# Performance work log

Measured on AMD Instinct MI355X. Metric: run time of the kernel, lower is better.

## Reference

```python
import jax, jax.numpy as jnp
import numpy as np

IMG = 640
C = 256
A = 9
NC = 80
K = 1000          # max candidates kept into NMS (fixed for jit)
SCORE_TH = 0.05
IOU_TH = 0.5
STRIDES = (8, 16, 32, 64, 128)
SIZES = (32, 64, 128, 256, 512)


def conv3(x, w, b):
    # x: [N,C,H,W], w: [O,I,3,3]
    y = jax.lax.conv_general_dilated(x, w, (1, 1), 'SAME',
                                     dimension_numbers=('NCHW', 'OIHW', 'NCHW'))
    return y + b[None, :, None, None]


def head(x, ws, bs, hw, hb):
    for i in range(4):
        x = jax.nn.relu(conv3(x, ws[i], bs[i]))
    return conv3(x, hw, hb)


def classifier(x, ws, bs, hw, hb):
    y = jax.nn.sigmoid(head(x, ws, bs, hw, hb))          # [N, A*NC, H, W]
    n, _, h, w = y.shape
    y = y.transpose(0, 2, 3, 1).reshape(n, h, w, A, NC)  # NHWA,NC ordering as in torch view
    return y.reshape(n, -1, NC)


def regressor(x, ws, bs, hw, hb):
    y = head(x, ws, bs, hw, hb)                           # [N, A*4, H, W]
    n, _, h, w = y.shape
    return y.transpose(0, 2, 3, 1).reshape(n, -1, 4)


def make_anchors():
    ratios = jnp.array([0.5, 1.0, 2.0], jnp.float32)
    scales = jnp.array([1.0, 2.0 ** (1.0 / 3.0), 2.0 ** (2.0 / 3.0)], jnp.float32)
    levels = []
    for stride, size in zip(STRIDES, SIZES):
        ws = (size * scales[None, :]) / jnp.sqrt(ratios[:, None])  # [3,3]
        hs = (size * scales[None, :]) * jnp.sqrt(ratios[:, None])
        ws, hs = ws.reshape(-1), hs.reshape(-1)                    # [9]
        fs = IMG // stride
        c = (jnp.arange(fs, dtype=jnp.float32) + 0.5) * stride
        cy, cx = jnp.meshgrid(c, c, indexing='ij')                 # [H,W]
        cx, cy = cx[..., None], cy[..., None]                      # [H,W,1]
        boxes = jnp.stack([cx - ws / 2, cy - hs / 2, cx + ws / 2, cy + hs / 2], -1)  # [H,W,9,4]
        levels.append(boxes.reshape(-1, 4))
    return jnp.concatenate(levels, 0)  # [76725, 4]


def decode_clip(anchors, loc):
    # BBoxTransform with std (0.1,0.1,0.2,0.2), then ClipBoxes to image
    w = anchors[:, 2] - anchors[:, 0]
    h = anchors[:, 3] - anchors[:, 1]
    cx = anchors[:, 0] + 0.5 * w
    cy = anchors[:, 1] + 0.5 * h
    dx, dy = loc[:, 0] * 0.1, loc[:, 1] * 0.1
    dw, dh = loc[:, 2] * 0.2, loc[:, 3] * 0.2
    pcx, pcy = cx + dx * w, cy + dy * h
    pw, ph = jnp.exp(dw) * w, jnp.exp(dh) * h
    boxes = jnp.stack([pcx - 0.5 * pw, pcy - 0.5 * ph, pcx + 0.5 * pw, pcy + 0.5 * ph], -1)
    return jnp.clip(boxes, 0.0, float(IMG))


def nms_keep(boxes, valid):
    # boxes [K,4] sorted by descending score, valid [K] bool; greedy NMS keep mask
    x1, y1, x2, y2 = boxes[:, 0], boxes[:, 1], boxes[:, 2], boxes[:, 3]
    area = jnp.maximum(x2 - x1, 0.0) * jnp.maximum(y2 - y1, 0.0)
    xx1 = jnp.maximum(x1[:, None], x1[None, :])
    yy1 = jnp.maximum(y1[:, None], y1[None, :])
    xx2 = jnp.minimum(x2[:, None], x2[None, :])
    yy2 = jnp.minimum(y2[:, None], y2[None, :])
    inter = jnp.maximum(xx2 - xx1, 0.0) * jnp.maximum(yy2 - yy1, 0.0)
    iou = inter / (area[:, None] + area[None, :] - inter + 1e-8)
    idx = jnp.arange(boxes.shape[0])

    def body(i, keep):
        sup = (iou[i] > IOU_TH) & (idx > i) & keep[i]
        return keep & ~sup

    return jax.lax.fori_loop(0, boxes.shape[0], body, valid)


def forward(p3, p4, p5, p6, p7, cls_w, cls_b, cls_hw, cls_hb, reg_w, reg_b, reg_hw, reg_hb):
    feats = [p3, p4, p5, p6, p7]
    cls_pred = jnp.concatenate([classifier(f, cls_w, cls_b, cls_hw, cls_hb) for f in feats], 1)[0]  # [N_anch, NC]
    loc_pred = jnp.concatenate([regressor(f, reg_w, reg_b, reg_hw, reg_hb) for f in feats], 1)[0]   # [N_anch, 4]
    anchors = make_anchors()
    boxes = decode_clip(anchors, loc_pred)
    scores = jnp.max(cls_pred, axis=1)                     # [N_anch]
    masked = jnp.where(scores > SCORE_TH, scores, -1.0)
    top_vals, top_idx = jax.lax.top_k(masked, K)
    valid = top_vals > 0.0
    sel_boxes = boxes[top_idx]                             # [K,4]
    keep = nms_keep(sel_boxes, valid)
    sel_cls = cls_pred[top_idx]                            # [K,NC]
    nms_scores = jnp.where(keep, top_vals, 0.0)
    nms_classes = jnp.argmax(sel_cls, axis=1).astype(jnp.int32)
    nms_boxes = jnp.where(keep[:, None], sel_boxes, 0.0)
    return nms_scores, nms_classes, nms_boxes, keep


def setup_inputs() -> dict:
    key = jax.random.key(0)
    ks = jax.random.split(key, 12)
    inp = {}
    for i, (name, hw_) in enumerate(zip(['p3', 'p4', 'p5', 'p6', 'p7'], [80, 40, 20, 10, 5])):
        inp[name] = jax.random.normal(ks[i], (1, C, hw_, hw_), jnp.float32)
    inp['cls_w'] = jax.random.normal(ks[5], (4, C, C, 3, 3), jnp.float32) * 0.05
    inp['cls_b'] = jnp.zeros((4, C), jnp.float32)
    inp['cls_hw'] = jax.random.normal(ks[6], (A * NC, C, 3, 3), jnp.float32) * 0.05
    inp['cls_hb'] = jnp.full((A * NC,), -2.0, jnp.float32)
    inp['reg_w'] = jax.random.normal(ks[7], (4, C, C, 3, 3), jnp.float32) * 0.05
    inp['reg_b'] = jnp.zeros((4, C), jnp.float32)
    inp['reg_hw'] = jax.random.normal(ks[8], (36, C, 3, 3), jnp.float32) * 0.05
    inp['reg_hb'] = jnp.zeros((36,), jnp.float32)
    return inp


def reference(p3, p4, p5, p6, p7, cls_w, cls_b, cls_hw, cls_hb, reg_w, reg_b, reg_hw, reg_hb):
    return forward(p3, p4, p5, p6, p7, cls_w, cls_b, cls_hw, cls_hb, reg_w, reg_b, reg_hw, reg_hb)
```

## Files before the change

kernel.cpp:

```cpp
#include <hip/hip_runtime.h>
#include <math.h>
#include <stdint.h>

#define NANCH 76725
#define NPAD  131072
#define NPAD2 32768
#define PXTOT 8525

typedef _Float16 half8 __attribute__((ext_vector_type(8)));
typedef _Float16 half4 __attribute__((ext_vector_type(4)));
typedef float float4v __attribute__((ext_vector_type(4)));
typedef unsigned long long u64;

#define ACT2_EL  ((size_t)PXTOT * 512)
#define HEADC_EL (720 * PXTOT)
#define HEADR_EL (36 * PXTOT)

#define TRUNK_WP_EL (9 * 2 * 8 * 16 * 64 * 8)
#define CLSH_WP_EL  (9 * 2 * 8 * 48 * 64 * 8)
#define REGH_WP_EL  (9 * 2 * 8 * 4 * 64 * 8)

struct PrepArgs {
    const float* src[10];
    _Float16*    dst[10];
    int Co[10], NC16[10];
    long base[11];
};

__global__ __launch_bounds__(256) void prep_k(PrepArgs P)
{
    long idx = (long)blockIdx.x * 256 + threadIdx.x;
    if (idx >= P.base[10]) return;
    int e = 0;
    while (idx >= P.base[e + 1]) e++;
    long local = idx - P.base[e];
    const int NC16 = P.NC16[e], Co = P.Co[e];
    int lane = (int)(local & 63);
    long t2 = local >> 6;
    int c16 = (int)(t2 % NC16);
    long t3 = t2 / NC16;
    int cc = (int)(t3 & 7);
    int t4 = (int)(t3 >> 3);
    int s = t4 & 1, tap = t4 >> 1;
    int co = c16 * 16 + (lane & 15);
    int kb = cc * 32 + (lane >> 4) * 8;
    const float* src = P.src[e];
    half8 out;
#pragma unroll
    for (int j = 0; j < 8; j++) {
        float v = (co < Co) ? src[(size_t)(co * 256 + kb + j) * 9 + tap] : 0.f;
        _Float16 h = (_Float16)v;
        out[j] = s ? (_Float16)(v - (float)h) : h;
    }
    _Float16* dst = P.dst[e] + ((((size_t)(tap * 2 + s) * 8 + cc) * NC16 + c16) * 64 + lane) * 8;
    *(half8*)dst = out;
}

struct RepArgs { const float* src[5]; _Float16* dst; };

__global__ __launch_bounds__(256) void repack_k(RepArgs R)
{
    __shared__ float T[64][257];
    const int cumT[5] = {100, 125, 132, 134, 135};
    const int Wt[5]   = {80, 40, 20, 10, 5};
    const int pxB[5]  = {0, 6400, 8000, 8400, 8500};
    int t = blockIdx.x;
    int lv = 0; while (t >= cumT[lv]) lv++;
    int tile = t - (lv ? cumT[lv - 1] : 0);
    const int HW = Wt[lv] * Wt[lv];
    const int pxStart = tile * 64;
    const float* src = R.src[lv];
    const int tid = threadIdx.x, w = tid >> 6, l6 = tid & 63;
    int p = pxStart + l6;
    bool ok = p < HW;
    for (int ci = w; ci < 256; ci += 4)
        T[l6][ci] = ok ? src[(size_t)ci * HW + p] : 0.f;
    __syncthreads();
    _Float16* dst = R.dst + (size_t)pxB[lv] * 512;
    for (int px = w; px < 64; px += 4) {
        int pp = pxStart + px;
        if (pp >= HW) continue;
        half4 h, l;
#pragma unroll
        for (int j = 0; j < 4; j++) {
            float v = T[px][l6 * 4 + j];
            _Float16 hh = (_Float16)v;
            h[j] = hh; l[j] = (_Float16)(v - (float)hh);
        }
        *(half4*)(dst + (size_t)pp * 512 + l6 * 4) = h;
        *(half4*)(dst + (size_t)pp * 512 + 256 + l6 * 4) = l;
    }
}

struct C3Args {
    const _Float16* aIn0; const _Float16* aIn1;
    _Float16* aOut0; _Float16* aOut1;
    float* hOut0; float* hOut1;
    const _Float16* wp0; const _Float16* wp1;
    const float* bias0; const float* bias1;
    int CoPad0, CoPad1, Co0, Co1, mode;
};

__global__ __launch_bounds__(256, 4) void conv3_k(C3Args A)
{
    const int cumT[5] = {200, 250, 265, 271, 273};
    const int txA[5]  = {10, 5, 3, 2, 1};
    const int Wt[5]   = {80, 40, 20, 10, 5};
    const int pxB[5]  = {0, 6400, 8000, 8400, 8500};

    __shared__ __align__(16) _Float16 Xs[60 * 72];

    const int gid = blockIdx.x;
    int head, coGrp, t;
    if (A.mode == 0) {
        int oct = gid & 7; head = oct >> 2; int tq = oct & 3;
        int p = gid >> 3; coGrp = p & 1; int tl = p >> 1;
        t = tq * 69 + tl;
    } else {
        int oct = gid & 7; int tq = oct & 3; int ch = oct >> 2;
        int p = gid >> 3; int ci = p & 3; int tl = p >> 2;
        int combo = ch * 4 + ci;
        if (combo >= 7) return;
        head = (combo == 6) ? 1 : 0;
        coGrp = (combo == 6) ? 0 : combo;
        t = tq * 69 + tl;
    }
    if (t >= 273) return;

    int lv = 0; while (t >= cumT[lv]) lv++;
    const int tile = t - (lv ? cumT[lv - 1] : 0);
    const int W = Wt[lv], HW = W * W;
    const int tx = txA[lv];
    const int tyi = tile / tx, txi = tile - tyi * tx;
    const int x0 = txi * 8, y0 = tyi * 4;

    const _Float16* aIn = (head ? A.aIn1 : A.aIn0) + (size_t)pxB[lv] * 512;
    const _Float16* wp  = head ? A.wp1 : A.wp0;
    const float* bias   = head ? A.bias1 : A.bias0;
    const int CoPad     = head ? A.CoPad1 : A.CoPad0;
    const int Co        = head ? A.Co1 : A.Co0;
    const int NC16      = CoPad >> 4;

    const int tid = threadIdx.x;
    const int w = tid >> 6, lane = tid & 63;
    const int l15 = lane & 15, quad = lane >> 4;
    const int coW = coGrp * 128 + w * 32;
    const bool active = coW < CoPad;
    const int c16b = coW >> 4;

    float4v acc[2][2];
#pragma unroll
    for (int i = 0; i < 2; i++)
#pragma unroll
        for (int j = 0; j < 2; j++) acc[i][j] = (float4v){0.f, 0.f, 0.f, 0.f};

    const half8 z8 = {(_Float16)0, (_Float16)0, (_Float16)0, (_Float16)0,
                      (_Float16)0, (_Float16)0, (_Float16)0, (_Float16)0};

    for (int cc = 0; cc < 8; cc++) {
        const int ci0 = cc * 32;
        __syncthreads();
        {
            int u0 = tid, u1 = tid + 256;
            int px0 = u0 >> 3, sg0 = u0 & 7;
            int r0 = px0 / 10, c0 = px0 - r0 * 10;
            int gy0 = y0 + r0 - 1, gx0 = x0 + c0 - 1;
            bool v0ok = (gy0 >= 0) && (gy0 < W) && (gx0 >= 0) && (gx0 < W);
            int e0 = (sg0 < 4) ? (ci0 + sg0 * 8) : (256 + ci0 + (sg0 - 4) * 8);
            int gp0 = v0ok ? (gy0 * W + gx0) : 0;
            half8 v0 = v0ok ? *(const half8*)(aIn + (size_t)gp0 * 512 + e0) : z8;

            bool u1v = u1 < 480;
            int px1 = u1 >> 3, sg1 = u1 & 7;
            int r1 = px1 / 10, c1 = px1 - r1 * 10;
            int gy1 = y0 + r1 - 1, gx1 = x0 + c1 - 1;
            bool v1ok = u1v && (gy1 >= 0) && (gy1 < W) && (gx1 >= 0) && (gx1 < W);
            int e1 = (sg1 < 4) ? (ci0 + sg1 * 8) : (256 + ci0 + (sg1 - 4) * 8);
            int gp1 = v1ok ? (gy1 * W + gx1) : 0;
            half8 v1 = v1ok ? *(const half8*)(aIn + (size_t)gp1 * 512 + e1) : z8;

            *(half8*)(Xs + px0 * 72 + sg0 * 8) = v0;
            if (u1v) *(half8*)(Xs + px1 * 72 + sg1 * 8) = v1;
        }
        __syncthreads();

        if (active) {
            for (int tap = 0; tap < 9; tap++) {
                const int dy = tap / 3 - 1, dx = tap % 3 - 1;
                half8 ah[2], al[2];
#pragma unroll
                for (int mf = 0; mf < 2; mf++) {
                    int lpx = (2 * mf + (l15 >> 3) + 1 + dy) * 10 + (l15 & 7) + 1 + dx;
                    const _Float16* lp = Xs + lpx * 72 + quad * 8;
                    ah[mf] = *(const half8*)lp;
                    al[mf] = *(const half8*)(lp + 32);
                }
                half8 bh[2], bl[2];
#pragma unroll
                for (int nf = 0; nf < 2; nf++) {
                    const _Float16* wb = wp +
                        ((((size_t)(tap * 2) * 8 + cc) * NC16 + c16b + nf) * 64 + lane) * 8;
                    bh[nf] = *(const half8*)wb;
                    bl[nf] = *(const half8*)(wb + (size_t)4096 * NC16);
                }
#pragma unroll
                for (int nf = 0; nf < 2; nf++) {
#pragma unroll
                    for (int mf = 0; mf < 2; mf++) {
                        acc[mf][nf] = __builtin_amdgcn_mfma_f32_16x16x32_f16(ah[mf], bh[nf], acc[mf][nf], 0, 0, 0);
                        acc[mf][nf] = __builtin_amdgcn_mfma_f32_16x16x32_f16(ah[mf], bl[nf], acc[mf][nf], 0, 0, 0);
                        acc[mf][nf] = __builtin_amdgcn_mfma_f32_16x16x32_f16(al[mf], bh[nf], acc[mf][nf], 0, 0, 0);
                    }
                }
            }
        }
    }

    if (!active) return;

    int coN[2];
    float bv[2];
#pragma unroll
    for (int nf = 0; nf < 2; nf++) {
        coN[nf] = coW + nf * 16 + l15;
        bv[nf] = (coN[nf] < Co) ? bias[coN[nf]] : 0.f;
    }

    if (A.mode == 0) {
        _Float16* ao = (head ? A.aOut1 : A.aOut0) + (size_t)pxB[lv] * 512;
#pragma unroll
        for (int nf = 0; nf < 2; nf++) {
#pragma unroll
            for (int mf = 0; mf < 2; mf++) {
#pragma unroll
                for (int r = 0; r < 4; r++) {
                    int m = quad * 4 + r;
                    int yy = y0 + 2 * mf + (m >> 3);
                    int xx = x0 + (m & 7);
                    if (yy < W && xx < W) {
                        int px = yy * W + xx;
                        float v = fmaxf(acc[mf][nf][r] + bv[nf], 0.f);
                        _Float16 h = (_Float16)v;
                        _Float16 lo = (_Float16)(v - (float)h);
                        ao[(size_t)px * 512 + coN[nf]] = h;
                        ao[(size_t)px * 512 + 256 + coN[nf]] = lo;
                    }
                }
            }
        }
    } else {
        float* ho = (head ? A.hOut1 : A.hOut0) + (size_t)Co * pxB[lv];
#pragma unroll
        for (int nf = 0; nf < 2; nf++) {
            if (coN[nf] < Co) {
                float* col = ho + (size_t)coN[nf] * HW;
#pragma unroll
                for (int mf = 0; mf < 2; mf++) {
#pragma unroll
                    for (int r = 0; r < 4; r++) {
                        int m = quad * 4 + r;
                        int yy = y0 + 2 * mf + (m >> 3);
                        int xx = x0 + (m & 7);
                        if (yy < W && xx < W) col[yy * W + xx] = acc[mf][nf][r] + bv[nf];
                    }
                }
            }
        }
    }
}

__global__ void cls_reduce_k(const float* __restrict__ ho,
                             u64* __restrict__ keys, int* __restrict__ cls_all)
{
    const int cumB[5] = {225, 282, 297, 301, 302};
    const int HWs[5]  = {6400, 1600, 400, 100, 25};
    const int pxB[5]  = {0, 6400, 8000, 8400, 8500};
    const int offs[5] = {0, 57600, 72000, 75600, 76500};
    int b = blockIdx.x;
    int lv = 0;
    while (b >= cumB[lv]) lv++;
    int local = (b - (lv ? cumB[lv - 1] : 0)) * 256 + threadIdx.x;
    const int HW = HWs[lv];
    if (local >= HW * 9) return;
    int a = local / HW, p = local - a * HW;
    const float* base = ho + (size_t)720 * pxB[lv] + (size_t)a * 80 * HW + p;
    float m = -1.f; int arg = 0;
    for (int c = 0; c < 80; c++) {
        float logit = base[(size_t)c * HW];
        float s = 1.0f / (1.0f + expf(-logit));
        if (s > m) { m = s; arg = c; }
    }
    float masked = (m > 0.05f) ? m : -1.0f;
    unsigned u = __float_as_uint(masked);
    unsigned su = (u & 0x80000000u) ? ~u : (u | 0x80000000u);
    int g = offs[lv] + p * 9 + a;
    keys[g] = ((u64)su << 32) | (u64)(0xFFFFFFFFu - (unsigned)g);
    cls_all[g] = arg;
}

struct DecArgs { float aw[45]; float ah[45]; };

__global__ void decode_k(const float* __restrict__ ro, DecArgs D, float* __restrict__ boxes_all)
{
    const int cumB[5] = {225, 282, 297, 301, 302};
    const int HWs[5]  = {6400, 1600, 400, 100, 25};
    const int Wt[5]   = {80, 40, 20, 10, 5};
    const int pxB[5]  = {0, 6400, 8000, 8400, 8500};
    const int offs[5] = {0, 57600, 72000, 75600, 76500};
    const float strd[5] = {8.f, 16.f, 32.f, 64.f, 128.f};
    int b = blockIdx.x;
    int lv = 0;
    while (b >= cumB[lv]) lv++;
    int local = (b - (lv ? cumB[lv - 1] : 0)) * 256 + threadIdx.x;
    const int HW = HWs[lv], W = Wt[lv];
    if (local >= HW * 9) return;
    int a = local / HW, p = local - a * HW;
    int y = p / W, x = p - y * W;
    float cx0 = ((float)x + 0.5f) * strd[lv];
    float cy0 = ((float)y + 0.5f) * strd[lv];
    float aw = D.aw[lv * 9 + a], ahh = D.ah[lv * 9 + a];
    float ax1 = cx0 - aw * 0.5f, ax2 = cx0 + aw * 0.5f;
    float ay1 = cy0 - ahh * 0.5f, ay2 = cy0 + ahh * 0.5f;
    float w = ax2 - ax1, h = ay2 - ay1;
    float cx = ax1 + 0.5f * w, cy = ay1 + 0.5f * h;
    const float* base = ro + (size_t)36 * pxB[lv] + p;
    float l0 = base[(size_t)(a * 4 + 0) * HW];
    float l1 = base[(size_t)(a * 4 + 1) * HW];
    float l2 = base[(size_t)(a * 4 + 2) * HW];
    float l3 = base[(size_t)(a * 4 + 3) * HW];
    float dx = l0 * 0.1f, dy = l1 * 0.1f, dw = l2 * 0.2f, dh = l3 * 0.2f;
    float pcx = cx + dx * w, pcy = cy + dy * h;
    float pw = expf(dw) * w, ph = expf(dh) * h;
    float bx1 = fminf(fmaxf(pcx - 0.5f * pw, 0.f), 640.f);
    float by1 = fminf(fmaxf(pcy - 0.5f * ph, 0.f), 640.f);
    float bx2 = fminf(fmaxf(pcx + 0.5f * pw, 0.f), 640.f);
    float by2 = fminf(fmaxf(pcy + 0.5f * ph, 0.f), 640.f);
    int g = offs[lv] + p * 9 + a;
    boxes_all[g * 4 + 0] = bx1;
    boxes_all[g * 4 + 1] = by1;
    boxes_all[g * 4 + 2] = bx2;
    boxes_all[g * 4 + 3] = by2;
}

__global__ void pad_keys_k(u64* __restrict__ keys)
{
    int i = blockIdx.x * blockDim.x + threadIdx.x + NANCH;
    if (i < NPAD) keys[i] = 0ULL;
}

__global__ __launch_bounds__(1024) void chunk_sort_desc_k(u64* __restrict__ keys)
{
    __shared__ u64 s[4096];
    const int base = blockIdx.x * 4096;
    for (int i = threadIdx.x; i < 4096; i += 1024) s[i] = keys[base + i];
    __syncthreads();
    for (int size = 2; size <= 4096; size <<= 1) {
        for (int stride = size >> 1; stride > 0; stride >>= 1) {
            for (int t = threadIdx.x; t < 2048; t += 1024) {
                int low = t & (stride - 1);
                int i = ((t - low) << 1) | low;
                int j = i + stride;
                bool desc = ((i & size) == 0);
                u64 a = s[i], b = s[j];
                if (desc ? (a < b) : (a > b)) { s[i] = b; s[j] = a; }
            }
            __syncthreads();
        }
    }
    for (int i = threadIdx.x; i < 4096; i += 1024) keys[base + i] = s[i];
}

__global__ __launch_bounds__(1024) void gather_top_k(const u64* __restrict__ keys,
                                                     u64* __restrict__ keys2)
{
    int i = blockIdx.x * 1024 + threadIdx.x;
    keys2[i] = keys[(i >> 10) * 4096 + (i & 1023)];
}

__global__ void bitonic_global_k(u64* __restrict__ keys, int size, int stride)
{
    int t = blockIdx.x * blockDim.x + threadIdx.x;
    int low = t & (stride - 1);
    int i = ((t - low) << 1) | low;
    int j = i + stride;
    bool desc = ((i & size) == 0);
    u64 a = keys[i], b = keys[j];
    if (desc ? (a < b) : (a > b)) { keys[i] = b; keys[j] = a; }
}

__global__ __launch_bounds__(1024) void bitonic_local_full_k(u64* __restrict__ keys)
{
    __shared__ u64 s[4096];
    const int base = blockIdx.x * 4096;
    for (int i = threadIdx.x; i < 4096; i += 1024) s[i] = keys[base + i];
    __syncthreads();
    for (int size = 2; size <= 4096; size <<= 1) {
        for (int stride = size >> 1; stride > 0; stride >>= 1) {
            for (int t = threadIdx.x; t < 2048; t += 1024) {
                int low = t & (stride - 1);
                int i = ((t - low) << 1) | low;
                int j = i + stride;
                bool desc = (((base + i) & size) == 0);
                u64 a = s[i], b = s[j];
                if (desc ? (a < b) : (a > b)) { s[i] = b; s[j] = a; }
            }
            __syncthreads();
        }
    }
    for (int i = threadIdx.x; i < 4096; i += 1024) keys[base + i] = s[i];
}

__global__ __launch_bounds__(1024) void bitonic_local_k(u64* __restrict__ keys, int size)
{
    __shared__ u64 s[4096];
    const int base = blockIdx.x * 4096;
    for (int i = threadIdx.x; i < 4096; i += 1024) s[i] = keys[base + i];
    __syncthreads();
    const bool desc = ((base & size) == 0);
    for (int stride = 2048; stride > 0; stride >>= 1) {
        for (int t = threadIdx.x; t < 2048; t += 1024) {
            int low = t & (stride - 1);
            int i = ((t - low) << 1) | low;
            int j = i + stride;
            u64 a = s[i], b = s[j];
            if (desc ? (a < b) : (a > b)) { s[i] = b; s[j] = a; }
        }
        __syncthreads();
    }
    for (int i = threadIdx.x; i < 4096; i += 1024) keys[base + i] = s[i];
}

__global__ void gather_cand_k(const u64* __restrict__ keys,
                              const float* __restrict__ boxes_all,
                              const int* __restrict__ cls_all,
                              float* __restrict__ cand)
{
    int i = blockIdx.x * 256 + threadIdx.x;
    if (i >= 1000) return;
    u64 k = keys[i];
    unsigned shi = (unsigned)(k >> 32);
    unsigned u = (shi & 0x80000000u) ? (shi ^ 0x80000000u) : ~shi;
    float val = __uint_as_float(u);
    int anchor = (int)(0xFFFFFFFFu - (unsigned)(k & 0xFFFFFFFFull));
    float x1 = boxes_all[anchor * 4 + 0];
    float y1 = boxes_all[anchor * 4 + 1];
    float x2 = boxes_all[anchor * 4 + 2];
    float y2 = boxes_all[anchor * 4 + 3];
    cand[i * 8 + 0] = x1;
    cand[i * 8 + 1] = y1;
    cand[i * 8 + 2] = x2;
    cand[i * 8 + 3] = y2;
    cand[i * 8 + 4] = fmaxf(x2 - x1, 0.f) * fmaxf(y2 - y1, 0.f);
    cand[i * 8 + 5] = val;
    cand[i * 8 + 6] = (float)cls_all[anchor];
    cand[i * 8 + 7] = (val > 0.0f) ? 1.f : 0.f;
}

__global__ __launch_bounds__(256) void iou_mask_k(const float* __restrict__ cand,
                                                  u64* __restrict__ mask)
{
    const int i = blockIdx.x;
    const float x1 = cand[i * 8 + 0], y1 = cand[i * 8 + 1];
    const float x2 = cand[i * 8 + 2], y2 = cand[i * 8 + 3];
    const float ar = cand[i * 8 + 4];
    const int tid = threadIdx.x;
    const int wave = tid >> 6, lane = tid & 63;
    for (int base = 0; base < 1024; base += 256) {
        int j = base + tid;
        bool sup = false;
        if (j < 1000 && j > i) {
            float jx1 = cand[j * 8 + 0], jy1 = cand[j * 8 + 1];
            float jx2 = cand[j * 8 + 2], jy2 = cand[j * 8 + 3];
            float jar = cand[j * 8 + 4];
            float xx1 = fmaxf(x1, jx1), yy1 = fmaxf(y1, jy1);
            float xx2 = fminf(x2, jx2), yy2 = fminf(y2, jy2);
            float inter = fmaxf(xx2 - xx1, 0.f) * fmaxf(yy2 - yy1, 0.f);
            float iou = inter / (ar + jar - inter + 1e-8f);
            sup = iou > 0.5f;
        }
        u64 ball = __ballot(sup);
        int word = (base >> 6) + wave;
        if (lane == 0) mask[(size_t)i * 16 + word] = ball;
    }
}

__global__ __launch_bounds__(256) void nms_sweep_out_k(const float* __restrict__ cand,
                                                       const u64* __restrict__ M,
                                                       float* __restrict__ out)
{
    __shared__ float C[1000 * 8];
    __shared__ int KPs[1000];
    const int tid = threadIdx.x;
    for (int i = tid; i < 8000; i += 256) C[i] = cand[i];
    __syncthreads();

    if (tid < 64) {
        const int l = tid;
        u64 s = 0;
        u64 cur = M[l];
        for (int base = 0; base < 1000; base += 4) {
            u64 nxt = 0;
            if (base + 8 <= 1000) nxt = M[(base + 4) * 16 + l];
#pragma unroll
            for (int k = 0; k < 4; k++) {
                int i = base + k;
                u64 sw = __shfl(s, i >> 6);
                bool alive = (C[i * 8 + 7] > 0.f) && !((sw >> (i & 63)) & 1);
                u64 rw = __shfl(cur, k * 16 + (l & 15));
                if (alive && l < 16) s |= rw;
                if (l == 0) KPs[i] = alive ? 1 : 0;
            }
            cur = nxt;
        }
    }
    __syncthreads();

    for (int i = tid; i < 1000; i += 256) {
        int kp = KPs[i];
        float m = kp ? 1.f : 0.f;
        out[i] = kp ? C[i * 8 + 5] : 0.f;
        out[1000 + i] = C[i * 8 + 6];
        out[2000 + i * 4 + 0] = m * C[i * 8 + 0];
        out[2000 + i * 4 + 1] = m * C[i * 8 + 1];
        out[2000 + i * 4 + 2] = m * C[i * 8 + 2];
        out[2000 + i * 4 + 3] = m * C[i * 8 + 3];
        out[6000 + i] = m;
    }
}

extern "C" void kernel_launch(void* const* d_in, const int* in_sizes, int n_in,
                              void* d_out, int out_size, void* d_ws, size_t ws_size,
                              hipStream_t stream)
{
    const float* feats[5];
    for (int i = 0; i < 5; i++) feats[i] = (const float*)d_in[i];
    const float* cls_w  = (const float*)d_in[5];
    const float* cls_b  = (const float*)d_in[6];
    const float* cls_hw = (const float*)d_in[7];
    const float* cls_hb = (const float*)d_in[8];
    const float* reg_w  = (const float*)d_in[9];
    const float* reg_b  = (const float*)d_in[10];
    const float* reg_hw = (const float*)d_in[11];
    const float* reg_hb = (const float*)d_in[12];
    float* out = (float*)d_out;

    char* ws = (char*)d_ws;
    size_t off = 0;
    auto alloc = [&](size_t sz) { size_t o = off; off += (sz + 255) & ~(size_t)255; return o; };

    size_t R0 = alloc((size_t)(HEADC_EL + HEADR_EL) * 4);
    _Float16* act2_feats = (_Float16*)(ws + R0);
    float* headout_cls = (float*)(ws + R0);
    float* headout_reg = headout_cls + HEADC_EL;

    _Float16* a2_clsA = (_Float16*)(ws + alloc(ACT2_EL * 2));
    _Float16* a2_regA = (_Float16*)(ws + alloc(ACT2_EL * 2));
    _Float16* a2_clsB = (_Float16*)(ws + alloc(ACT2_EL * 2));
    _Float16* a2_regB = (_Float16*)(ws + alloc(ACT2_EL * 2));

    _Float16* wpc[4]; _Float16* wpr[4];
    for (int i = 0; i < 4; i++) wpc[i] = (_Float16*)(ws + alloc((size_t)TRUNK_WP_EL * 2));
    _Float16* wpch = (_Float16*)(ws + alloc((size_t)CLSH_WP_EL * 2));
    for (int i = 0; i < 4; i++) wpr[i] = (_Float16*)(ws + alloc((size_t)TRUNK_WP_EL * 2));
    _Float16* wprh = (_Float16*)(ws + alloc((size_t)REGH_WP_EL * 2));

    u64* keys  = (u64*)(ws + alloc((size_t)NPAD * 8));
    u64* keys2 = (u64*)(ws + alloc((size_t)NPAD2 * 8));
    float* boxes_all = (float*)(ws + alloc((size_t)NANCH * 16));
    int* cls_all = (int*)(ws + alloc((size_t)NANCH * 4));
    float* cand = (float*)(ws + alloc((size_t)1000 * 8 * 4));
    u64* mask = (u64*)(ws + alloc((size_t)1000 * 16 * 8));
    (void)ws_size;

    PrepArgs P;
    long cum = 0;
    for (int e = 0; e < 10; e++) {
        const float* src; _Float16* dst; int Co, NC16;
        if (e < 4)      { src = cls_w + (size_t)e * 589824; dst = wpc[e]; Co = 256; NC16 = 16; }
        else if (e == 4){ src = cls_hw;                     dst = wpch;   Co = 720; NC16 = 48; }
        else if (e < 9) { src = reg_w + (size_t)(e - 5) * 589824; dst = wpr[e - 5]; Co = 256; NC16 = 16; }
        else            { src = reg_hw;                     dst = wprh;   Co = 36;  NC16 = 4; }
        P.src[e] = src; P.dst[e] = dst; P.Co[e] = Co; P.NC16[e] = NC16;
        P.base[e] = cum; cum += (long)9216 * NC16;
    }
    P.base[10] = cum;
    prep_k<<<(int)((cum + 255) / 256), 256, 0, stream>>>(P);

    pad_keys_k<<<(NPAD - NANCH + 255) / 256, 256, 0, stream>>>(keys);

    RepArgs R;
    for (int lv = 0; lv < 5; lv++) R.src[lv] = feats[lv];
    R.dst = act2_feats;
    repack_k<<<135, 256, 0, stream>>>(R);

    auto trunk = [&](const _Float16* i0, const _Float16* i1, _Float16* o0, _Float16* o1,
                     const _Float16* w0, const _Float16* w1, const float* b0, const float* b1) {
        C3Args C;
        C.aIn0 = i0; C.aIn1 = i1; C.aOut0 = o0; C.aOut1 = o1;
        C.hOut0 = nullptr; C.hOut1 = nullptr;
        C.wp0 = w0; C.wp1 = w1; C.bias0 = b0; C.bias1 = b1;
        C.CoPad0 = 256; C.CoPad1 = 256;
        C.Co0 = 256; C.Co1 = 256; C.mode = 0;
        conv3_k<<<8 * 2 * 69, 256, 0, stream>>>(C);
    };
    trunk(act2_feats, act2_feats, a2_clsA, a2_regA, wpc[0], wpr[0], cls_b + 0,   reg_b + 0);
    trunk(a2_clsA,    a2_regA,    a2_clsB, a2_regB, wpc[1], wpr[1], cls_b + 256, reg_b + 256);
    trunk(a2_clsB,    a2_regB,    a2_clsA, a2_regA, wpc[2], wpr[2], cls_b + 512, reg_b + 512);
    trunk(a2_clsA,    a2_regA,    a2_clsB, a2_regB, wpc[3], wpr[3], cls_b + 768, reg_b + 768);

    {
        C3Args C;
        C.aIn0 = a2_clsB; C.aIn1 = a2_regB;
        C.aOut0 = nullptr; C.aOut1 = nullptr;
        C.hOut0 = headout_cls; C.hOut1 = headout_reg;
        C.wp0 = wpch; C.wp1 = wprh; C.bias0 = cls_hb; C.bias1 = reg_hb;
        C.CoPad0 = 768; C.CoPad1 = 64;
        C.Co0 = 720; C.Co1 = 36; C.mode = 1;
        conv3_k<<<8 * 4 * 69, 256, 0, stream>>>(C);
    }

    cls_reduce_k<<<302, 256, 0, stream>>>(headout_cls, keys, cls_all);

    DecArgs D;
    {
        const float sz[5] = {32.f, 64.f, 128.f, 256.f, 512.f};
        const float ratios[3] = {0.5f, 1.0f, 2.0f};
        const float scales[3] = {1.0f, 1.25992104989487316477f, 1.58740105196819947475f};
        for (int lv = 0; lv < 5; lv++)
            for (int r = 0; r < 3; r++)
                for (int s = 0; s < 3; s++) {
                    D.aw[lv * 9 + r * 3 + s] = sz[lv] * scales[s] / sqrtf(ratios[r]);
                    D.ah[lv * 9 + r * 3 + s] = sz[lv] * scales[s] * sqrtf(ratios[r]);
                }
    }
    decode_k<<<302, 256, 0, stream>>>(headout_reg, D, boxes_all);

    chunk_sort_desc_k<<<NPAD / 4096, 1024, 0, stream>>>(keys);
    gather_top_k<<<NPAD2 / 1024, 1024, 0, stream>>>(keys, keys2);
    bitonic_local_full_k<<<NPAD2 / 4096, 1024, 0, stream>>>(keys2);
    for (int size = 8192; size <= NPAD2; size <<= 1) {
        for (int stride = size >> 1; stride >= 4096; stride >>= 1)
            bitonic_global_k<<<NPAD2 / 2 / 1024, 1024, 0, stream>>>(keys2, size, stride);
        bitonic_local_k<<<NPAD2 / 4096, 1024, 0, stream>>>(keys2, size);
    }

    gather_cand_k<<<4, 256, 0, stream>>>(keys2, boxes_all, cls_all, cand);
    iou_mask_k<<<1000, 256, 0, stream>>>(cand, mask);
    nms_sweep_out_k<<<1, 256, 0, stream>>>(cand, mask, out);
}
```

Measured before the change: 917.6 us.

## Restructure NMS sweep into blocked 64-row tiles with wave-level OR reductions

Replaces the serial per-candidate NMS sweep, which loads mask words from global memory in a dependent chain, with a tiled scheme. Each 64-candidate tile is resolved inside one wave by shuffling row masks. Suppression for later tiles is then pushed forward with butterfly OR reductions over the rows that survived. Shared-memory staging of candidates is removed and the kernel runs as a single 64-thread wave, aiming to shorten the serial dependency chain. This adds many shuffle reductions and register arrays, which may spill, and the sweep is still only a small part of the total runtime.

```diff
diff --git a/kernel.cpp b/kernel.cpp
--- a/kernel.cpp
+++ b/kernel.cpp
@@ -484,46 +484,60 @@
     }
 }
 
-__global__ __launch_bounds__(256) void nms_sweep_out_k(const float* __restrict__ cand,
-                                                       const u64* __restrict__ M,
-                                                       float* __restrict__ out)
-{
-    __shared__ float C[1000 * 8];
-    __shared__ int KPs[1000];
-    const int tid = threadIdx.x;
-    for (int i = tid; i < 8000; i += 256) C[i] = cand[i];
-    __syncthreads();
-
-    if (tid < 64) {
-        const int l = tid;
-        u64 s = 0;
-        u64 cur = M[l];
-        for (int base = 0; base < 1000; base += 4) {
-            u64 nxt = 0;
-            if (base + 8 <= 1000) nxt = M[(base + 4) * 16 + l];
-#pragma unroll
-            for (int k = 0; k < 4; k++) {
-                int i = base + k;
-                u64 sw = __shfl(s, i >> 6);
-                bool alive = (C[i * 8 + 7] > 0.f) && !((sw >> (i & 63)) & 1);
-                u64 rw = __shfl(cur, k * 16 + (l & 15));
-                if (alive && l < 16) s |= rw;
-                if (l == 0) KPs[i] = alive ? 1 : 0;
-            }
-            cur = nxt;
-        }
-    }
-    __syncthreads();
-
-    for (int i = tid; i < 1000; i += 256) {
-        int kp = KPs[i];
+__global__ __launch_bounds__(64) void nms_sweep_out_k(const float* __restrict__ cand,
+                                                      const u64* __restrict__ M,
+                                                      float* __restrict__ out)
+{
+    const int lane = threadIdx.x;
+
+    u64 V[16];
+#pragma unroll
+    for (int t = 0; t < 16; t++) {
+        int i = t * 64 + lane;
+        bool v = (i < 1000) && (cand[i * 8 + 7] > 0.f);
+        V[t] = __ballot(v);
+    }
+
+    u64 pend[16];
+#pragma unroll
+    for (int t = 0; t < 16; t++) pend[t] = 0;
+    u64 aliveW[16];
+
+    for (int T = 0; T < 16; T++) {
+        u64 rw[16];
+        int row = T * 64 + lane;
+        for (int t = T; t < 16; t++)
+            rw[t] = (row < 1000) ? M[(size_t)row * 16 + t] : 0ULL;
+
+        u64 s = pend[T];
+        u64 alive = 0;
+        u64 myw = rw[T];
+        const u64 VT = V[T];
+#pragma unroll
+        for (int i = 0; i < 64; i++) {
+            u64 ri = __shfl(myw, i);
+            bool a = ((VT >> i) & 1) && !((s >> i) & 1);
+            if (a) { s |= ri; alive |= (1ULL << i); }
+        }
+        aliveW[T] = alive;
+
+        for (int t = T + 1; t < 16; t++) {
+            u64 c = ((alive >> lane) & 1) ? rw[t] : 0ULL;
+#pragma unroll
+            for (int d = 1; d < 64; d <<= 1) c |= __shfl_xor(c, d);
+            pend[t] |= c;
+        }
+    }
+
+    for (int i = lane; i < 1000; i += 64) {
+        int kp = (int)((aliveW[i >> 6] >> (i & 63)) & 1);
         float m = kp ? 1.f : 0.f;
-        out[i] = kp ? C[i * 8 + 5] : 0.f;
-        out[1000 + i] = C[i * 8 + 6];
-        out[2000 + i * 4 + 0] = m * C[i * 8 + 0];
-        out[2000 + i * 4 + 1] = m * C[i * 8 + 1];
-        out[2000 + i * 4 + 2] = m * C[i * 8 + 2];
-        out[2000 + i * 4 + 3] = m * C[i * 8 + 3];
+        out[i] = kp ? cand[i * 8 + 5] : 0.f;
+        out[1000 + i] = cand[i * 8 + 6];
+        out[2000 + i * 4 + 0] = m * cand[i * 8 + 0];
+        out[2000 + i * 4 + 1] = m * cand[i * 8 + 1];
+        out[2000 + i * 4 + 2] = m * cand[i * 8 + 2];
+        out[2000 + i * 4 + 3] = m * cand[i * 8 + 3];
         out[6000 + i] = m;
     }
 }
@@ -646,5 +660,5 @@
 
     gather_cand_k<<<4, 256, 0, stream>>>(keys2, boxes_all, cls_all, cand);
     iou_mask_k<<<1000, 256, 0, stream>>>(cand, mask);
-    nms_sweep_out_k<<<1, 256, 0, stream>>>(cand, mask, out);
-}
+    nms_sweep_out_k<<<1, 64, 0, stream>>>(cand, mask, out);
+}
```

New measurement: 864.2 us. 1.06x faster.
